# Optimization experiments

Hardware: AMD Instinct MI355X
Metric: run time of the kernel (lower is better)

Reference implementation:

```python
import jax, jax.numpy as jnp
from jax import lax
import numpy as np


def conv2d(x, w, b, stride, pad):
    # x: [B,C,H,W], w: [O,I,kh,kw]
    y = lax.conv_general_dilated(x, w, (stride, stride), [(pad, pad), (pad, pad)],
                                 dimension_numbers=('NCHW', 'OIHW', 'NCHW'))
    return y + b[None, :, None, None]


def gru_cell(x, h, zr_w, zr_b, h_w, h_b):
    # standard ConvGRU cell, kernel 5 pad 2
    zr = jax.nn.sigmoid(conv2d(jnp.concatenate([x, h], axis=1), zr_w, zr_b, 1, 2))
    z, r = jnp.split(zr, 2, axis=1)
    h_tilde = jnp.tanh(conv2d(jnp.concatenate([x, r * h], axis=1), h_w, h_b, 1, 2))
    return (1.0 - z) * h + z * h_tilde


def stage(xs, h0, cw, cb, zrw, zrb, hw, hb):
    # xs: [T,B,C,H,W] time-major; strided conv (k4,s2,p1) then ConvGRU per step
    def step(h, x):
        xt = conv2d(x, cw, cb, 2, 1)
        hn = gru_cell(xt, h, zrw, zrb, hw, hb)
        return hn, hn
    hT, hs = lax.scan(step, h0, xs)
    return hT, hs


def _mk_params(key):
    h1, h2, h3, cin = 64, 128, 128, 1
    ks = jax.random.split(key, 9)
    s = 0.05
    p = {}
    p['c1_w'] = jax.random.normal(ks[0], (h1, cin, 4, 4), jnp.float32) * s
    p['c1_b'] = jnp.zeros((h1,), jnp.float32)
    p['g1_zr_w'] = jax.random.normal(ks[1], (2 * h1, 2 * h1, 5, 5), jnp.float32) * s
    p['g1_zr_b'] = jnp.zeros((2 * h1,), jnp.float32)
    p['g1_h_w'] = jax.random.normal(ks[2], (h1, 2 * h1, 5, 5), jnp.float32) * s
    p['g1_h_b'] = jnp.zeros((h1,), jnp.float32)
    p['c2_w'] = jax.random.normal(ks[3], (h2, h1, 4, 4), jnp.float32) * s
    p['c2_b'] = jnp.zeros((h2,), jnp.float32)
    p['g2_zr_w'] = jax.random.normal(ks[4], (2 * h2, 2 * h2, 5, 5), jnp.float32) * s
    p['g2_zr_b'] = jnp.zeros((2 * h2,), jnp.float32)
    p['g2_h_w'] = jax.random.normal(ks[5], (h2, 2 * h2, 5, 5), jnp.float32) * s
    p['g2_h_b'] = jnp.zeros((h2,), jnp.float32)
    p['c3_w'] = jax.random.normal(ks[6], (h3, h2, 4, 4), jnp.float32) * s
    p['c3_b'] = jnp.zeros((h3,), jnp.float32)
    p['g3_zr_w'] = jax.random.normal(ks[7], (2 * h3, 2 * h3, 5, 5), jnp.float32) * s
    p['g3_zr_b'] = jnp.zeros((2 * h3,), jnp.float32)
    p['g3_h_w'] = jax.random.normal(ks[8], (h3, 2 * h3, 5, 5), jnp.float32) * s
    p['g3_h_b'] = jnp.zeros((h3,), jnp.float32)
    return p


def setup_inputs() -> dict:
    key = jax.random.key(0)
    k_in, k_p = jax.random.split(key)
    inp = {'input': jax.random.normal(k_in, (8, 12, 1, 128, 128), jnp.float32)}
    inp.update(_mk_params(k_p))
    return inp


def reference(input, c1_w, c1_b, g1_zr_w, g1_zr_b, g1_h_w, g1_h_b,
              c2_w, c2_b, g2_zr_w, g2_zr_b, g2_h_w, g2_h_b,
              c3_w, c3_b, g3_zr_w, g3_zr_b, g3_h_w, g3_h_b):
    B, T, C, H, W = input.shape
    h1, h2, h3 = g1_h_w.shape[0], g2_h_w.shape[0], g3_h_w.shape[0]
    xs = jnp.transpose(input, (1, 0, 2, 3, 4))  # [T,B,C,H,W]
    s1 = jnp.zeros((B, h1, H // 2, W // 2), input.dtype)
    state1, seq1 = stage(xs, s1, c1_w, c1_b, g1_zr_w, g1_zr_b, g1_h_w, g1_h_b)
    s2 = jnp.zeros((B, h2, H // 4, W // 4), input.dtype)
    state2, seq2 = stage(seq1, s2, c2_w, c2_b, g2_zr_w, g2_zr_b, g2_h_w, g2_h_b)
    s3 = jnp.zeros((B, h3, H // 8, W // 8), input.dtype)
    state3, _ = stage(seq2, s3, c3_w, c3_b, g3_zr_w, g3_zr_b, g3_h_w, g3_h_b)
    return (state1, state2, state3)
```

## Files before the change

kernel.cpp:

```cpp
#include <hip/hip_runtime.h>
#include <math.h>

typedef _Float16 f16;
typedef __attribute__((ext_vector_type(8))) _Float16 half8;
typedef __attribute__((ext_vector_type(4))) float f32x4;

static __device__ __forceinline__ float sigmoid_f(float x) { return 1.0f / (1.0f + expf(-x)); }

static __device__ __forceinline__ void splitf(float x, f16& hi, f16& lo) {
    hi = (f16)x;
    float r = x - (float)hi;
    lo = (f16)(r * 4096.0f);
}

template <int KH, int KW, int KPT, int MODE, int NG, int NOC, int D,
          int CBI, int KB0, int WPI, int PIXPI,
          int WSH, int HWOUT, int OC, int STRIDE, int POFF,
          int CBO, int OCH0, int WPO, int PIXPO>
static __device__ __forceinline__ void gemm_conv_body(
    int bx, int by, int b,
    const f16* Ah, const f16* Al, const f16* __restrict__ Wt,
    const float* __restrict__ bias, const float* __restrict__ zbuf,
    float* zout, f16* Oh, f16* Ol, f16* smem)
{
    constexpr int NSTEP = KH * KW * KPT;
    constexpr int WOUT  = 1 << WSH;
    constexpr int OCB   = OC / 16;
    constexpr int STG   = 4;
    constexpr int NGRP  = NSTEP / STG;
    constexpr int PPW   = (STG * NOC) / 4;
    static_assert(NSTEP % STG == 0, "NSTEP divisible by STG");
    static_assert(STG % D == 0, "D must divide STG");
    static_assert(NOC == 2 || NOC == 4, "NOC in {2,4}");

    const int lane = threadIdx.x & 63;
    const int wave = threadIdx.x >> 6;
    const int pixbase = (bx * 4 + wave) * (NG * 16);
    const int ocbase  = by * (NOC * 16);

    const f16* ph[NG];
    const f16* pl[NG];
#pragma unroll
    for (int g = 0; g < NG; ++g) {
        int apix = pixbase + 16 * g + (lane & 15);
        int y = apix >> WSH, x = apix & (WOUT - 1);
        int p0 = (y * STRIDE + POFF) * WPI + (x * STRIDE + POFF);
        size_t o = ((size_t)(b * CBI + KB0) * PIXPI + p0) * 32 + (lane >> 4) * 8;
        ph[g] = Ah + o;
        pl[g] = Al + o;
    }

    int lk = 0, lkx = 0;
    auto advance = [&]() {
#pragma unroll
        for (int g = 0; g < NG; ++g) { ph[g] += (size_t)PIXPI * 32; pl[g] += (size_t)PIXPI * 32; }
        if (++lk == KPT) {
            lk = 0;
            int shift = 1;
            if (++lkx == KW) { lkx = 0; shift = WPI - (KW - 1); }
            const long ad = (long)shift * 32 - (long)KPT * PIXPI * 32;
#pragma unroll
            for (int g = 0; g < NG; ++g) { ph[g] += ad; pl[g] += ad; }
        }
    };

    auto bpiece = [&](int s, int j) -> const f16* {
        int t = s / KPT, kb = s % KPT;
        return Wt + (((size_t)(t * OCB + by * NOC + j)) * KPT + kb) * 512;
    };

    half8 stg[PPW];
    auto stage_issue = [&](int g0) {
#pragma unroll
        for (int p = 0; p < PPW; ++p) {
            const int pc = wave * PPW + p;
            const int kk = pc / NOC, j = pc % NOC;
            stg[p] = *(const half8*)(bpiece(g0 * STG + kk, j) + lane * 8);
        }
    };
    auto stage_write = [&](f16* dst) {
#pragma unroll
        for (int p = 0; p < PPW; ++p) {
            const int pc = wave * PPW + p;
            *(half8*)(dst + pc * 512 + lane * 8) = stg[p];
        }
    };

    half8 bh[D][NG], bl[D][NG];
    half8 bwreg[2][NOC];
    f32x4 acc[NG][NOC] = {};
    f32x4 acc2[NG][NOC] = {};

    stage_issue(0);
    stage_write(smem);
#pragma unroll
    for (int s = 0; s < D - 1; ++s) {
#pragma unroll
        for (int g = 0; g < NG; ++g) {
            bh[s][g] = *(const half8*)ph[g];
            bl[s][g] = *(const half8*)pl[g];
        }
        advance();
    }
    asm volatile("s_waitcnt lgkmcnt(0)" ::: "memory");
    __builtin_amdgcn_s_barrier();
    __builtin_amdgcn_sched_barrier(0);

#pragma unroll 1
    for (int gi = 0; gi < NGRP; ++gi) {
        f16* cur = smem + (gi & 1) * 8192;
        f16* nxt = smem + ((gi & 1) ^ 1) * 8192;
        if (gi + 1 < NGRP) stage_issue(gi + 1);
#pragma unroll
        for (int j = 0; j < NOC; ++j)
            bwreg[0][j] = *(const half8*)(cur + j * 512 + lane * 8);
#pragma unroll
        for (int kk = 0; kk < STG; ++kk) {
            if (kk + 1 < STG) {
#pragma unroll
                for (int j = 0; j < NOC; ++j)
                    bwreg[(kk + 1) & 1][j] = *(const half8*)(cur + ((kk + 1) * NOC + j) * 512 + lane * 8);
            }
            const int ls = (kk + D - 1) % D;
#pragma unroll
            for (int g = 0; g < NG; ++g) {
                bh[ls][g] = *(const half8*)ph[g];
                bl[ls][g] = *(const half8*)pl[g];
            }
            advance();
            const int dd = kk % D;
#pragma unroll
            for (int j = 0; j < NOC; ++j)
#pragma unroll
                for (int g = 0; g < NG; ++g) {
                    acc[g][j]  = __builtin_amdgcn_mfma_f32_16x16x32_f16(bh[dd][g], bwreg[kk & 1][j], acc[g][j], 0, 0, 0);
                    acc2[g][j] = __builtin_amdgcn_mfma_f32_16x16x32_f16(bl[dd][g], bwreg[kk & 1][j], acc2[g][j], 0, 0, 0);
                }
        }
        if (gi + 1 < NGRP) {
            stage_write(nxt);
            asm volatile("s_waitcnt lgkmcnt(0)" ::: "memory");
            __builtin_amdgcn_s_barrier();
            __builtin_amdgcn_sched_barrier(0);
        }
    }

    constexpr int Cc = (MODE == 0) ? (OC >> 1) : OC;
#pragma unroll
    for (int g = 0; g < NG; ++g) {
#pragma unroll
        for (int j = 0; j < NOC; ++j) {
            const int oc = ocbase + j * 16 + (lane & 15);
            const float bv = bias[oc];
#pragma unroll
            for (int r = 0; r < 4; ++r) {
                const int pix = pixbase + 16 * g + ((lane >> 4) << 2) + r;
                const int y = pix >> WSH, x = pix & (WOUT - 1);
                const int pr = (y + 2) * WPI + (x + 2);
                const int pwr = (y + 2) * WPO + (x + 2);
                const size_t pz = (size_t)b * HWOUT + pix;
                float a = acc[g][j][r] + acc2[g][j][r] * (1.0f / 4096.0f) + bv;
                if (MODE == 0) {
                    float s = sigmoid_f(a);
                    if (oc < Cc) {
                        zout[pz * Cc + oc] = s;
                    } else {
                        int hch = oc - Cc;
                        size_t hidx = ((size_t)(b * CBI + (hch >> 5)) * PIXPI + pr) * 32 + (hch & 31);
                        float hv = (float)Ah[hidx] + (float)Al[hidx] * (1.0f / 4096.0f);
                        float rh = s * hv;
                        f16 hi, lo; splitf(rh, hi, lo);
                        int wch = Cc + oc;
                        size_t widx = ((size_t)(b * CBO + (wch >> 5)) * PIXPO + pwr) * 32 + (wch & 31);
                        Oh[widx] = hi; Ol[widx] = lo;
                    }
                } else if (MODE == 1) {
                    size_t hidx = ((size_t)(b * CBI + (oc >> 5)) * PIXPI + pr) * 32 + (oc & 31);
                    float hv = (float)Ah[hidx] + (float)Al[hidx] * (1.0f / 4096.0f);
                    float zv = zbuf[pz * Cc + oc];
                    float hn = (1.f - zv) * hv + zv * tanhf(a);
                    f16 hi, lo; splitf(hn, hi, lo);
                    Oh[hidx] = hi; Ol[hidx] = lo;
                } else {
                    f16 hi, lo; splitf(a, hi, lo);
                    int wch = OCH0 + oc;
                    size_t widx = ((size_t)(b * CBO + (wch >> 5)) * PIXPO + pwr) * 32 + (wch & 31);
                    Oh[widx] = hi; Ol[widx] = lo;
                }
            }
        }
    }
}

static __device__ __forceinline__ void conv1_body(
    int bx, int b,
    const float* __restrict__ in, const float* __restrict__ w,
    const float* __restrict__ bias, f16* Oh, f16* Ol)
{
    const int tid = threadIdx.x;
    const int px  = bx * 64 + (tid & 63);
    const int ocg = tid >> 6;
    const int y = px >> 6, x = px & 63;
    const float* src = in + (size_t)b * 196608;
    float v[16];
#pragma unroll
    for (int ky = 0; ky < 4; ++ky)
#pragma unroll
        for (int kx = 0; kx < 4; ++kx) {
            int iy = 2 * y - 1 + ky, ix = 2 * x - 1 + kx;
            v[ky * 4 + kx] = ((unsigned)iy < 128u && (unsigned)ix < 128u) ? src[iy * 128 + ix] : 0.f;
        }
    const int p = (y + 2) * 68 + (x + 2);
#pragma unroll
    for (int o = 0; o < 16; ++o) {
        int ch = 64 + ocg * 16 + o;
        float s = bias[ch - 64];
        const float* wr = w + (ch - 64) * 16;
#pragma unroll
        for (int t = 0; t < 16; ++t) s += wr[t] * v[t];
        f16 hi, lo; splitf(s, hi, lo);
        size_t idx = ((size_t)(b * 6 + (ch >> 5)) * 4624 + p) * 32 + (ch & 31);
        Oh[idx] = hi; Ol[idx] = lo;
    }
}


__global__ __launch_bounds__(256) void fused_L1(
    const float* __restrict__ input, const float* __restrict__ c1w, const float* __restrict__ c1b,
    f16* cat1h, f16* cat1l,
    const f16* __restrict__ wt_c2, const float* __restrict__ c2b, f16* cat2h, f16* cat2l,
    const f16* __restrict__ wt_c3, const float* __restrict__ c3b, f16* cat3h, f16* cat3l,
    int t1, int a2, int a3)
{
    __shared__ f16 smem[2 * 8192];
    const int lin = blockIdx.x;
    if (lin < 256) {
        if (!a2) return;
        gemm_conv_body<4, 4, 2, 2, 1, 4, 4, 6, 0, 68, 4624, 5, 1024, 128, 2, 1, 12, 128, 36, 1296>(
            lin & 15, (lin >> 4) & 1, lin >> 5,
            cat1h, cat1l, wt_c2, c2b, nullptr, nullptr, cat2h, cat2l, smem);
    } else if (lin < 384) {
        if (!a3) return;
        const int l = lin - 256;
        gemm_conv_body<4, 4, 4, 2, 1, 2, 4, 12, 0, 36, 1296, 4, 256, 128, 2, 1, 12, 128, 20, 400>(
            l & 3, (l >> 2) & 3, l >> 4,
            cat2h, cat2l, wt_c3, c3b, nullptr, nullptr, cat3h, cat3l, smem);
    } else {
        if (t1 < 0) return;
        const int l = lin - 384;
        conv1_body(l & 63, l >> 6, input + (size_t)t1 * 16384, c1w, c1b, cat1h, cat1l);
    }
}

__global__ __launch_bounds__(256) void fused_L2(
    f16* cat1h, f16* cat1l, const f16* __restrict__ wt_g1zr, const float* __restrict__ g1zrb, float* z1,
    f16* cat2h, f16* cat2l, const f16* __restrict__ wt_g2zr, const float* __restrict__ g2zrb, float* z2,
    f16* cat3h, f16* cat3l, const f16* __restrict__ wt_g3zr, const float* __restrict__ g3zrb, float* z3,
    int a1, int a2, int a3)
{
    __shared__ f16 smem[2 * 8192];
    const int lin = blockIdx.x;
    if (lin < 512) {
        if (!a1) return;
        gemm_conv_body<5, 5, 4, 0, 2, 4, 2, 6, 0, 68, 4624, 6, 4096, 128, 1, 0, 6, 0, 68, 4624>(
            lin & 31, (lin >> 5) & 1, lin >> 6,
            cat1h, cat1l, wt_g1zr, g1zrb, nullptr, z1, cat1h, cat1l, smem);
    } else if (lin < 1024) {
        if (!a2) return;
        const int l = lin - 512;
        gemm_conv_body<5, 5, 8, 0, 1, 4, 4, 12, 0, 36, 1296, 5, 1024, 256, 1, 0, 12, 0, 36, 1296>(
            l & 15, (l >> 4) & 3, l >> 6,
            cat2h, cat2l, wt_g2zr, g2zrb, nullptr, z2, cat2h, cat2l, smem);
    } else {
        if (!a3) return;
        const int l = lin - 1024;
        gemm_conv_body<5, 5, 8, 0, 1, 2, 4, 12, 0, 20, 400, 4, 256, 256, 1, 0, 12, 0, 20, 400>(
            l & 3, (l >> 2) & 7, l >> 5,
            cat3h, cat3l, wt_g3zr, g3zrb, nullptr, z3, cat3h, cat3l, smem);
    }
}

__global__ __launch_bounds__(256) void fused_L3(
    f16* cat1h, f16* cat1l, const f16* __restrict__ wt_g1h, const float* __restrict__ g1hb, const float* z1,
    f16* cat2h, f16* cat2l, const f16* __restrict__ wt_g2h, const float* __restrict__ g2hb, const float* z2,
    f16* cat3h, f16* cat3l, const f16* __restrict__ wt_g3h, const float* __restrict__ g3hb, const float* z3,
    int a1, int a2, int a3)
{
    __shared__ f16 smem[2 * 8192];
    const int lin = blockIdx.x;
    if (lin < 256) {
        if (!a2) return;
        gemm_conv_body<5, 5, 8, 1, 1, 4, 4, 12, 4, 36, 1296, 5, 1024, 128, 1, 0, 12, 0, 36, 1296>(
            lin & 15, (lin >> 4) & 1, lin >> 5,
            cat2h, cat2l, wt_g2h, g2hb, z2, nullptr, cat2h, cat2l, smem);
    } else if (lin < 768) {
        if (!a1) return;
        const int l = lin - 256;
        gemm_conv_body<5, 5, 4, 1, 1, 4, 4, 6, 2, 68, 4624, 6, 4096, 64, 1, 0, 6, 0, 68, 4624>(
            l & 63, 0, l >> 6,
            cat1h, cat1l, wt_g1h, g1hb, z1, nullptr, cat1h, cat1l, smem);
    } else {
        if (!a3) return;
        const int l = lin - 768;
        gemm_conv_body<5, 5, 8, 1, 1, 2, 4, 12, 4, 20, 400, 4, 256, 128, 1, 0, 12, 0, 20, 400>(
            l & 3, (l >> 2) & 3, l >> 4,
            cat3h, cat3l, wt_g3h, g3hb, z3, nullptr, cat3h, cat3l, smem);
    }
}

__global__ __launch_bounds__(256) void prep_w(
    const float* __restrict__ w, f16* __restrict__ wt,
    int OC, int IC, int KK, int perm)
{
    int i = blockIdx.x * 256 + threadIdx.x;
    int total = OC * IC * KK;
    if (i >= total) return;
    int oc = i / (IC * KK);
    int r  = i - oc * (IC * KK);
    int ic = r / KK;
    int tap = r - ic * KK;
    int icn = perm ? ((ic < IC / 2) ? ic + IC / 2 : ic - IC / 2) : ic;
    int OCB = OC >> 4, KPT = IC >> 5;
    int ob = oc >> 4, ol = oc & 15;
    int kb = icn >> 5, kg = (icn >> 3) & 3, ch = icn & 7;
    size_t o = (((size_t)tap * OCB + ob) * KPT + kb) * 512 + kg * 128 + ol * 8 + ch;
    wt[o] = (f16)w[i];
}

__global__ __launch_bounds__(256) void cat_to_nchw(
    const f16* __restrict__ hi, const f16* __restrict__ lo,
    float* __restrict__ dst, int C, int HW, int wsh, int WP, int PIXP, int CB)
{
    int i = blockIdx.x * 256 + threadIdx.x;
    int b = i / (C * HW);
    int r = i - b * (C * HW);
    int c = r / HW;
    int p = r - c * HW;
    int y = p >> wsh, x = p & ((1 << wsh) - 1);
    size_t s = ((size_t)(b * CB + (c >> 5)) * PIXP + (size_t)(y + 2) * WP + (x + 2)) * 32 + (c & 31);
    dst[i] = (float)hi[s] + (float)lo[s] * (1.0f / 4096.0f);
}

extern "C" void kernel_launch(void* const* d_in, const int* in_sizes, int n_in,
                              void* d_out, int out_size, void* d_ws, size_t ws_size,
                              hipStream_t stream)
{
    (void)in_sizes; (void)n_in; (void)out_size; (void)ws_size;

    const float* input  = (const float*)d_in[0];
    const float* c1_w   = (const float*)d_in[1];
    const float* c1_b   = (const float*)d_in[2];
    const float* g1zr_w = (const float*)d_in[3];
    const float* g1zr_b = (const float*)d_in[4];
    const float* g1h_w  = (const float*)d_in[5];
    const float* g1h_b  = (const float*)d_in[6];
    const float* c2_w   = (const float*)d_in[7];
    const float* c2_b   = (const float*)d_in[8];
    const float* g2zr_w = (const float*)d_in[9];
    const float* g2zr_b = (const float*)d_in[10];
    const float* g2h_w  = (const float*)d_in[11];
    const float* g2h_b  = (const float*)d_in[12];
    const float* c3_w   = (const float*)d_in[13];
    const float* c3_b   = (const float*)d_in[14];
    const float* g3zr_w = (const float*)d_in[15];
    const float* g3zr_b = (const float*)d_in[16];
    const float* g3h_w  = (const float*)d_in[17];
    const float* g3h_b  = (const float*)d_in[18];

    float* out1 = (float*)d_out;
    float* out2 = (float*)d_out + 2097152;
    float* out3 = (float*)d_out + 3145728;

    char* ws = (char*)d_ws;
    size_t off = 0;
    auto takeB = [&](size_t bytes) { char* p = ws + off; off += (bytes + 255) & ~(size_t)255; return p; };

    const size_t WSLACK = 400000;
    f16* wt_g1zr = (f16*)takeB((size_t)25 * 128 * 128 * 2 + WSLACK);
    f16* wt_g1h  = (f16*)takeB((size_t)25 * 64 * 128 * 2 + WSLACK);
    f16* wt_c2   = (f16*)takeB((size_t)16 * 128 * 64 * 2 + WSLACK);
    f16* wt_g2zr = (f16*)takeB((size_t)25 * 256 * 256 * 2 + WSLACK);
    f16* wt_g2h  = (f16*)takeB((size_t)25 * 128 * 256 * 2 + WSLACK);
    f16* wt_c3   = (f16*)takeB((size_t)16 * 128 * 128 * 2 + WSLACK);
    f16* wt_g3zr = (f16*)takeB((size_t)25 * 256 * 256 * 2 + WSLACK);
    f16* wt_g3h  = (f16*)takeB((size_t)25 * 128 * 256 * 2 + WSLACK);

    const size_t cat1_n = (size_t)8 * 6 * 4624 * 32;
    const size_t cat2_n = (size_t)8 * 12 * 1296 * 32;
    const size_t cat3_n = (size_t)8 * 12 * 400 * 32;
    const size_t ASLACK = 1 << 20;
    f16* cat1h = (f16*)takeB(cat1_n * 2 + ASLACK);
    f16* cat1l = (f16*)takeB(cat1_n * 2 + ASLACK);
    f16* cat2h = (f16*)takeB(cat2_n * 2 + ASLACK);
    f16* cat2l = (f16*)takeB(cat2_n * 2 + ASLACK);
    f16* cat3h = (f16*)takeB(cat3_n * 2 + ASLACK);
    f16* cat3l = (f16*)takeB(cat3_n * 2 + ASLACK);
    float* z1 = (float*)takeB((size_t)8 * 4096 * 64 * 4);
    float* z2 = (float*)takeB((size_t)8 * 1024 * 128 * 4);
    float* z3 = (float*)takeB((size_t)8 * 256 * 128 * 4);

    hipMemsetAsync(cat1h, 0, cat1_n * 2, stream);
    hipMemsetAsync(cat1l, 0, cat1_n * 2, stream);
    hipMemsetAsync(cat2h, 0, cat2_n * 2, stream);
    hipMemsetAsync(cat2l, 0, cat2_n * 2, stream);
    hipMemsetAsync(cat3h, 0, cat3_n * 2, stream);
    hipMemsetAsync(cat3l, 0, cat3_n * 2, stream);

    auto prep = [&](const float* w, f16* wt, int OC, int IC, int KK, int perm) {
        int total = OC * IC * KK;
        prep_w<<<(total + 255) / 256, 256, 0, stream>>>(w, wt, OC, IC, KK, perm);
    };
    prep(g1zr_w, wt_g1zr, 128, 128, 25, 1);
    prep(g1h_w,  wt_g1h,  64, 128, 25, 0);
    prep(c2_w,   wt_c2,   128, 64, 16, 0);
    prep(g2zr_w, wt_g2zr, 256, 256, 25, 1);
    prep(g2h_w,  wt_g2h,  128, 256, 25, 0);
    prep(c3_w,   wt_c3,   128, 128, 16, 0);
    prep(g3zr_w, wt_g3zr, 256, 256, 25, 1);
    prep(g3h_w,  wt_g3h,  128, 256, 25, 0);

    for (int i = 0; i < 14; ++i) {
        const int t1 = (i < 12) ? i : -1;
        const int a1 = (i < 12) ? 1 : 0;
        const int a2 = (i >= 1 && i <= 12) ? 1 : 0;
        const int a3 = (i >= 2) ? 1 : 0;

        fused_L1<<<896, 256, 0, stream>>>(
            input, c1_w, c1_b, cat1h, cat1l,
            wt_c2, c2_b, cat2h, cat2l,
            wt_c3, c3_b, cat3h, cat3l,
            t1, a2, a3);
        fused_L2<<<1280, 256, 0, stream>>>(
            cat1h, cat1l, wt_g1zr, g1zr_b, z1,
            cat2h, cat2l, wt_g2zr, g2zr_b, z2,
            cat3h, cat3l, wt_g3zr, g3zr_b, z3,
            a1, a2, a3);
        fused_L3<<<896, 256, 0, stream>>>(
            cat1h, cat1l, wt_g1h, g1h_b, z1,
            cat2h, cat2l, wt_g2h, g2h_b, z2,
            cat3h, cat3l, wt_g3h, g3h_b, z3,
            a1, a2, a3);
    }

    cat_to_nchw<<<8192, 256, 0, stream>>>(cat1h, cat1l, out1, 64, 4096, 6, 68, 4624, 6);
    cat_to_nchw<<<4096, 256, 0, stream>>>(cat2h, cat2l, out2, 128, 1024, 5, 36, 1296, 12);
    cat_to_nchw<<<1024, 256, 0, stream>>>(cat3h, cat3l, out3, 128, 256, 4, 20, 400, 12);
}
```

Before: 4.133 ms.

## Stage weights via direct global-to-LDS loads and deepen the GEMM pipeline

The conv GEMM body now copies weight tiles straight from global memory into LDS with global_load_lds, in place of going through registers and an LDS write, and waits on vmcnt instead of lgkmcnt. Stage size, load-ahead depth (D up to 8) and weight register lookahead (BAH) become template parameters, each conv picks its own values, and s_setprio is raised around the MFMA bursts. The g1 zr conv goes from two pixel groups per wave to one, so the L2 grid grows to 1792 blocks. The intent is to cut register pressure and LDS write traffic and to hide global latency better. The risks are more in-flight loads, more registers from the deeper D, and the new vmcnt counts being wrong.

```diff
diff --git a/kernel.cpp b/kernel.cpp
--- a/kernel.cpp
+++ b/kernel.cpp
@@ -4,6 +4,8 @@
 typedef _Float16 f16;
 typedef __attribute__((ext_vector_type(8))) _Float16 half8;
 typedef __attribute__((ext_vector_type(4))) float f32x4;
+
+template <int N> struct ic { static constexpr int v = N; };
 
 static __device__ __forceinline__ float sigmoid_f(float x) { return 1.0f / (1.0f + expf(-x)); }
 
@@ -13,7 +15,17 @@
     lo = (f16)(r * 4096.0f);
 }
 
-template <int KH, int KW, int KPT, int MODE, int NG, int NOC, int D,
+constexpr unsigned vmcnt_enc(int n) {
+    return (unsigned)((n & 15) | (7 << 4) | (15 << 8) | ((n >> 4) << 14));
+}
+
+static __device__ __forceinline__ void lds_stage16(const f16* src, f16* dst) {
+    typedef const __attribute__((address_space(1))) unsigned int* gup;
+    typedef __attribute__((address_space(3))) unsigned int* lup;
+    __builtin_amdgcn_global_load_lds((gup)(const void*)src, (lup)(void*)dst, 16, 0, 0);
+}
+
+template <int KH, int KW, int KPT, int MODE, int NG, int NOC, int D, int STG, int BAH,
           int CBI, int KB0, int WPI, int PIXPI,
           int WSH, int HWOUT, int OC, int STRIDE, int POFF,
           int CBO, int OCH0, int WPO, int PIXPO>
@@ -26,12 +38,15 @@
     constexpr int NSTEP = KH * KW * KPT;
     constexpr int WOUT  = 1 << WSH;
     constexpr int OCB   = OC / 16;
-    constexpr int STG   = 4;
     constexpr int NGRP  = NSTEP / STG;
+    constexpr int U     = (D > STG) ? (D / STG) : 1;
+    constexpr int NB    = BAH + 1;
     constexpr int PPW   = (STG * NOC) / 4;
-    static_assert(NSTEP % STG == 0, "NSTEP divisible by STG");
-    static_assert(STG % D == 0, "D must divide STG");
-    static_assert(NOC == 2 || NOC == 4, "NOC in {2,4}");
+    static_assert(NSTEP % STG == 0, "NSTEP % STG");
+    static_assert(NSTEP % D == 0, "NSTEP % D");
+    static_assert(U == 1 ? (STG % D == 0) : (D % STG == 0 && NGRP % U == 0), "phase");
+    static_assert(BAH >= 1 && BAH < STG, "BAH range");
+    static_assert(STG * NOC * 512 <= 8192, "group fits buffer");
 
     const int lane = threadIdx.x & 63;
     const int wave = threadIdx.x >> 6;
@@ -69,30 +84,21 @@
         return Wt + (((size_t)(t * OCB + by * NOC + j)) * KPT + kb) * 512;
     };
 
-    half8 stg[PPW];
-    auto stage_issue = [&](int g0) {
+    auto stage_lds = [&](int g0, f16* dst) {
 #pragma unroll
         for (int p = 0; p < PPW; ++p) {
             const int pc = wave * PPW + p;
             const int kk = pc / NOC, j = pc % NOC;
-            stg[p] = *(const half8*)(bpiece(g0 * STG + kk, j) + lane * 8);
+            lds_stage16(bpiece(g0 * STG + kk, j) + lane * 8, dst + pc * 512);
         }
     };
-    auto stage_write = [&](f16* dst) {
-#pragma unroll
-        for (int p = 0; p < PPW; ++p) {
-            const int pc = wave * PPW + p;
-            *(half8*)(dst + pc * 512 + lane * 8) = stg[p];
-        }
-    };
 
     half8 bh[D][NG], bl[D][NG];
-    half8 bwreg[2][NOC];
+    half8 bwreg[NB][NOC];
     f32x4 acc[NG][NOC] = {};
     f32x4 acc2[NG][NOC] = {};
 
-    stage_issue(0);
-    stage_write(smem);
+    stage_lds(0, smem);
 #pragma unroll
     for (int s = 0; s < D - 1; ++s) {
 #pragma unroll
@@ -102,47 +108,60 @@
         }
         advance();
     }
-    asm volatile("s_waitcnt lgkmcnt(0)" ::: "memory");
+    __builtin_amdgcn_s_waitcnt(vmcnt_enc((D - 1) * NG * 2));
+    asm volatile("" ::: "memory");
     __builtin_amdgcn_s_barrier();
     __builtin_amdgcn_sched_barrier(0);
 
-#pragma unroll 1
-    for (int gi = 0; gi < NGRP; ++gi) {
-        f16* cur = smem + (gi & 1) * 8192;
-        f16* nxt = smem + ((gi & 1) ^ 1) * 8192;
-        if (gi + 1 < NGRP) stage_issue(gi + 1);
-#pragma unroll
-        for (int j = 0; j < NOC; ++j)
-            bwreg[0][j] = *(const half8*)(cur + j * 512 + lane * 8);
+    auto group_body = [&](auto phc, int gi) __attribute__((always_inline)) {
+        constexpr int PH = decltype(phc)::v;
+        constexpr int PB = PH * STG;
+        const int par = (U == 2) ? PH : (gi & 1);
+        f16* cur = smem + par * 8192;
+        f16* nxt = smem + (par ^ 1) * 8192;
+        if (gi + 1 < NGRP) stage_lds(gi + 1, nxt);
+#pragma unroll
+        for (int q = 0; q < BAH; ++q)
+#pragma unroll
+            for (int j = 0; j < NOC; ++j)
+                bwreg[q % NB][j] = *(const half8*)(cur + (q * NOC + j) * 512 + lane * 8);
 #pragma unroll
         for (int kk = 0; kk < STG; ++kk) {
-            if (kk + 1 < STG) {
+            if (kk + BAH < STG) {
 #pragma unroll
                 for (int j = 0; j < NOC; ++j)
-                    bwreg[(kk + 1) & 1][j] = *(const half8*)(cur + ((kk + 1) * NOC + j) * 512 + lane * 8);
+                    bwreg[(kk + BAH) % NB][j] = *(const half8*)(cur + ((kk + BAH) * NOC + j) * 512 + lane * 8);
             }
-            const int ls = (kk + D - 1) % D;
+            const int ls = (PB + kk + D - 1) % D;
 #pragma unroll
             for (int g = 0; g < NG; ++g) {
                 bh[ls][g] = *(const half8*)ph[g];
                 bl[ls][g] = *(const half8*)pl[g];
             }
             advance();
-            const int dd = kk % D;
+            const int dd = (PB + kk) % D;
+            __builtin_amdgcn_s_setprio(1);
 #pragma unroll
             for (int j = 0; j < NOC; ++j)
 #pragma unroll
                 for (int g = 0; g < NG; ++g) {
-                    acc[g][j]  = __builtin_amdgcn_mfma_f32_16x16x32_f16(bh[dd][g], bwreg[kk & 1][j], acc[g][j], 0, 0, 0);
-                    acc2[g][j] = __builtin_amdgcn_mfma_f32_16x16x32_f16(bl[dd][g], bwreg[kk & 1][j], acc2[g][j], 0, 0, 0);
+                    acc[g][j]  = __builtin_amdgcn_mfma_f32_16x16x32_f16(bh[dd][g], bwreg[kk % NB][j], acc[g][j], 0, 0, 0);
+                    acc2[g][j] = __builtin_amdgcn_mfma_f32_16x16x32_f16(bl[dd][g], bwreg[kk % NB][j], acc2[g][j], 0, 0, 0);
                 }
+            __builtin_amdgcn_s_setprio(0);
         }
         if (gi + 1 < NGRP) {
-            stage_write(nxt);
-            asm volatile("s_waitcnt lgkmcnt(0)" ::: "memory");
+            __builtin_amdgcn_s_waitcnt(vmcnt_enc(STG * NG * 2));
+            asm volatile("" ::: "memory");
             __builtin_amdgcn_s_barrier();
             __builtin_amdgcn_sched_barrier(0);
         }
+    };
+
+#pragma unroll 1
+    for (int gi0 = 0; gi0 < NGRP; gi0 += U) {
+        group_body(ic<0>{}, gi0);
+        if constexpr (U == 2) group_body(ic<1>{}, gi0 + 1);
     }
 
     constexpr int Cc = (MODE == 0) ? (OC >> 1) : OC;
@@ -236,13 +255,13 @@
     const int lin = blockIdx.x;
     if (lin < 256) {
         if (!a2) return;
-        gemm_conv_body<4, 4, 2, 2, 1, 4, 4, 6, 0, 68, 4624, 5, 1024, 128, 2, 1, 12, 128, 36, 1296>(
+        gemm_conv_body<4, 4, 2, 2, 1, 4, 8, 4, 1, 6, 0, 68, 4624, 5, 1024, 128, 2, 1, 12, 128, 36, 1296>(
             lin & 15, (lin >> 4) & 1, lin >> 5,
             cat1h, cat1l, wt_c2, c2b, nullptr, nullptr, cat2h, cat2l, smem);
     } else if (lin < 384) {
         if (!a3) return;
         const int l = lin - 256;
-        gemm_conv_body<4, 4, 4, 2, 1, 2, 4, 12, 0, 36, 1296, 4, 256, 128, 2, 1, 12, 128, 20, 400>(
+        gemm_conv_body<4, 4, 4, 2, 1, 2, 8, 8, 2, 12, 0, 36, 1296, 4, 256, 128, 2, 1, 12, 128, 20, 400>(
             l & 3, (l >> 2) & 3, l >> 4,
             cat2h, cat2l, wt_c3, c3b, nullptr, nullptr, cat3h, cat3l, smem);
     } else {
@@ -261,20 +280,20 @@
     __shared__ f16 smem[2 * 8192];
     const int lin = blockIdx.x;
     if (lin < 512) {
+        if (!a2) return;
+        gemm_conv_body<5, 5, 8, 0, 1, 4, 8, 4, 1, 12, 0, 36, 1296, 5, 1024, 256, 1, 0, 12, 0, 36, 1296>(
+            lin & 15, (lin >> 4) & 3, lin >> 6,
+            cat2h, cat2l, wt_g2zr, g2zrb, nullptr, z2, cat2h, cat2l, smem);
+    } else if (lin < 1536) {
         if (!a1) return;
-        gemm_conv_body<5, 5, 4, 0, 2, 4, 2, 6, 0, 68, 4624, 6, 4096, 128, 1, 0, 6, 0, 68, 4624>(
-            lin & 31, (lin >> 5) & 1, lin >> 6,
+        const int l = lin - 512;
+        gemm_conv_body<5, 5, 4, 0, 1, 4, 4, 4, 2, 6, 0, 68, 4624, 6, 4096, 128, 1, 0, 6, 0, 68, 4624>(
+            l & 63, (l >> 6) & 1, l >> 7,
             cat1h, cat1l, wt_g1zr, g1zrb, nullptr, z1, cat1h, cat1l, smem);
-    } else if (lin < 1024) {
-        if (!a2) return;
-        const int l = lin - 512;
-        gemm_conv_body<5, 5, 8, 0, 1, 4, 4, 12, 0, 36, 1296, 5, 1024, 256, 1, 0, 12, 0, 36, 1296>(
-            l & 15, (l >> 4) & 3, l >> 6,
-            cat2h, cat2l, wt_g2zr, g2zrb, nullptr, z2, cat2h, cat2l, smem);
     } else {
         if (!a3) return;
-        const int l = lin - 1024;
-        gemm_conv_body<5, 5, 8, 0, 1, 2, 4, 12, 0, 20, 400, 4, 256, 256, 1, 0, 12, 0, 20, 400>(
+        const int l = lin - 1536;
+        gemm_conv_body<5, 5, 8, 0, 1, 2, 8, 8, 2, 12, 0, 20, 400, 4, 256, 256, 1, 0, 12, 0, 20, 400>(
             l & 3, (l >> 2) & 7, l >> 5,
             cat3h, cat3l, wt_g3zr, g3zrb, nullptr, z3, cat3h, cat3l, smem);
     }
@@ -290,19 +309,19 @@
     const int lin = blockIdx.x;
     if (lin < 256) {
         if (!a2) return;
-        gemm_conv_body<5, 5, 8, 1, 1, 4, 4, 12, 4, 36, 1296, 5, 1024, 128, 1, 0, 12, 0, 36, 1296>(
+        gemm_conv_body<5, 5, 8, 1, 1, 4, 8, 4, 1, 12, 4, 36, 1296, 5, 1024, 128, 1, 0, 12, 0, 36, 1296>(
             lin & 15, (lin >> 4) & 1, lin >> 5,
             cat2h, cat2l, wt_g2h, g2hb, z2, nullptr, cat2h, cat2l, smem);
     } else if (lin < 768) {
         if (!a1) return;
         const int l = lin - 256;
-        gemm_conv_body<5, 5, 4, 1, 1, 4, 4, 6, 2, 68, 4624, 6, 4096, 64, 1, 0, 6, 0, 68, 4624>(
+        gemm_conv_body<5, 5, 4, 1, 1, 4, 4, 4, 2, 6, 2, 68, 4624, 6, 4096, 64, 1, 0, 6, 0, 68, 4624>(
             l & 63, 0, l >> 6,
             cat1h, cat1l, wt_g1h, g1hb, z1, nullptr, cat1h, cat1l, smem);
     } else {
         if (!a3) return;
         const int l = lin - 768;
-        gemm_conv_body<5, 5, 8, 1, 1, 2, 4, 12, 4, 20, 400, 4, 256, 128, 1, 0, 12, 0, 20, 400>(
+        gemm_conv_body<5, 5, 8, 1, 1, 2, 8, 8, 2, 12, 4, 20, 400, 4, 256, 128, 1, 0, 12, 0, 20, 400>(
             l & 3, (l >> 2) & 3, l >> 4,
             cat3h, cat3l, wt_g3h, g3hb, z3, nullptr, cat3h, cat3l, smem);
     }
@@ -430,7 +449,7 @@
             wt_c2, c2_b, cat2h, cat2l,
             wt_c3, c3_b, cat3h, cat3l,
             t1, a2, a3);
-        fused_L2<<<1280, 256, 0, stream>>>(
+        fused_L2<<<1792, 256, 0, stream>>>(
             cat1h, cat1l, wt_g1zr, g1zr_b, z1,
             cat2h, cat2l, wt_g2zr, g2zr_b, z2,
             cat3h, cat3l, wt_g3zr, g3zr_b, z3,
```

Result: faster. 3.939 ms (-4.7%).
